# Performance work log

Measured on AMD Instinct MI355X. Metric: run time of the kernel, lower is better.

## Reference

```python
import jax, jax.numpy as jnp
import numpy as np

D_MODEL = 1024
H = 16
D_K = 64
D_V = 64
NEG_INF = -1e9
LN_EPS = 1e-5


def setup_inputs() -> dict:
    key = jax.random.key(0)
    ks = jax.random.split(key, 7)
    B, S = 4, 2048
    scale = 1.0 / np.sqrt(D_MODEL)
    return {
        "Q": jax.random.normal(ks[0], (B, S, D_MODEL), jnp.float32),
        "K": jax.random.normal(ks[1], (B, S, D_MODEL), jnp.float32),
        "V": jax.random.normal(ks[2], (B, S, D_MODEL), jnp.float32),
        "W_Q": jax.random.normal(ks[3], (D_MODEL, D_K * H), jnp.float32) * scale,
        "W_K": jax.random.normal(ks[4], (D_MODEL, D_K * H), jnp.float32) * scale,
        "W_V": jax.random.normal(ks[5], (D_MODEL, D_V * H), jnp.float32) * scale,
        "W_O": jax.random.normal(ks[6], (D_V * H, D_MODEL), jnp.float32) * scale,
        "ln_gamma": jnp.ones((D_MODEL,), jnp.float32),
        "ln_beta": jnp.zeros((D_MODEL,), jnp.float32),
    }


def reference(Q, K, V, W_Q, W_K, W_V, W_O, ln_gamma, ln_beta):
    B, Lq, _ = Q.shape
    Lk = K.shape[1]
    # projections, split into heads: [B, H, L, d]
    Qh = (Q @ W_Q).reshape(B, Lq, H, D_K).transpose(0, 2, 1, 3)
    Kh = (K @ W_K).reshape(B, Lk, H, D_K).transpose(0, 2, 1, 3)
    Vh = (V @ W_V).reshape(B, Lk, H, D_V).transpose(0, 2, 1, 3)
    # scaled dot-product scores [B, H, Lq, Lk]
    scores = jnp.einsum("bhqd,bhkd->bhqk", Qh, Kh) / jnp.sqrt(jnp.float32(D_K))
    # causal mask: upper triangle (excl. diagonal) gets -1e9 added
    mask = jnp.triu(jnp.full((Lq, Lk), NEG_INF, jnp.float32), k=1)
    scores = scores + mask
    attn = jax.nn.softmax(scores, axis=-1)
    ctx = jnp.einsum("bhqk,bhkd->bhqd", attn, Vh)
    ctx = ctx.transpose(0, 2, 1, 3).reshape(B, Lq, H * D_V)
    out = ctx @ W_O
    # residual + layernorm
    x = Q + out
    mu = jnp.mean(x, axis=-1, keepdims=True)
    var = jnp.mean(jnp.square(x - mu), axis=-1, keepdims=True)
    return (x - mu) * jax.lax.rsqrt(var + LN_EPS) * ln_gamma + ln_beta
```

## Files before the change

kernel.cpp:

```cpp
#include <hip/hip_runtime.h>
#include <cstdint>
#include <cstddef>

#define DM  1024
#define SEQ 2048
#define BATCH 4
#define NH  16
#define DH  64
#define QKS 2048

typedef __bf16 bf16_t;
typedef __bf16 bf16x8 __attribute__((ext_vector_type(8)));
typedef __bf16 bf16x4 __attribute__((ext_vector_type(4)));
typedef float  f32x4  __attribute__((ext_vector_type(4)));

#define MFMA16(a, b, c) __builtin_amdgcn_mfma_f32_16x16x32_bf16((a), (b), (c), 0, 0, 0)

#define CS 0.18033688f

#define ASYNC_COPY16(gsrc, ldst)                                                   \
  __builtin_amdgcn_global_load_lds(                                                \
      (__attribute__((address_space(1))) void*)(gsrc),                             \
      (__attribute__((address_space(3))) void*)(ldst), 16, 0, 0)

#define NCVT (3 * BATCH * SEQ * DM / 4 / 256)

__global__ __launch_bounds__(256) void prep_kernel(const float* __restrict__ Q,
                                                   const float* __restrict__ K,
                                                   const float* __restrict__ V,
                                                   const float* __restrict__ W0,
                                                   const float* __restrict__ W1,
                                                   const float* __restrict__ W2,
                                                   const float* __restrict__ W3,
                                                   bf16_t* __restrict__ Qb,
                                                   bf16_t* __restrict__ Kb,
                                                   bf16_t* __restrict__ Vb,
                                                   bf16_t* __restrict__ WTall) {
  __shared__ float tile[32][33];
  const int bid = blockIdx.x;
  if (bid < NCVT) {
    const int n4 = BATCH * SEQ * DM / 4;
    int i = bid * 256 + threadIdx.x;
    const float* src; bf16_t* dst; int j;
    if (i < n4)           { src = Q; dst = Qb; j = i; }
    else if (i < 2 * n4)  { src = K; dst = Kb; j = i - n4; }
    else                  { src = V; dst = Vb; j = i - 2 * n4; }
    float4 v = ((const float4*)src)[j];
    bf16x4 o;
    o[0] = (bf16_t)v.x; o[1] = (bf16_t)v.y; o[2] = (bf16_t)v.z; o[3] = (bf16_t)v.w;
    *(bf16x4*)(dst + (size_t)j * 4) = o;
    return;
  }
  const int wb = bid - NCVT;
  const int widx = wb >> 10, wid = wb & 1023;
  const float* W = (widx == 0) ? W0 : (widx == 1) ? W1 : (widx == 2) ? W2 : W3;
  bf16_t* WT = WTall + (size_t)widx * DM * DM;
  const int bn = wid & 31, bk = wid >> 5;
  const int tx = threadIdx.x & 31, ty = threadIdx.x >> 5;
#pragma unroll
  for (int r = 0; r < 4; ++r)
    tile[ty + r * 8][tx] = W[(size_t)(bk * 32 + ty + r * 8) * DM + bn * 32 + tx];
  __syncthreads();
#pragma unroll
  for (int r = 0; r < 4; ++r)
    WT[(size_t)(bn * 32 + ty + r * 8) * DM + bk * 32 + tx] = (bf16_t)tile[tx][ty + r * 8];
}

__global__ __launch_bounds__(256) void gemm_bt_kernel(const bf16_t* __restrict__ A0,
                                                      const bf16_t* __restrict__ A1,
                                                      const bf16_t* __restrict__ A2,
                                                      const bf16_t* __restrict__ BT,
                                                      bf16_t* __restrict__ C,
                                                      bf16_t* __restrict__ Vtr,
                                                      int K, int ldc,
                                                      float qscale, int qcols) {
  __shared__ bf16_t Sh[4][128 * 32];
  const int tid = threadIdx.x;
  const int wv = tid >> 6, lane = tid & 63;
  const int lo = lane & 15, quad = lane >> 4;

  const int bid = blockIdx.x;
  const int xcd = bid & 7;
  const int rid = bid >> 3;
  const int m0 = (xcd * 8 + (rid & 7)) * 128;
  const int n0 = (rid >> 3) * 128;
  const int wm = wv & 1, wn = wv >> 1;

  const bf16_t* A = (n0 < 1024) ? A0 : (n0 < 2048) ? A1 : A2;
  const float sc = (n0 < qcols) ? qscale : 1.0f;

  f32x4 acc[4][4] = {};

  const int srow = wv * 32 + (lane >> 2);
  const int scol = (lane & 3) * 8;
  const bf16_t* Ag = A + (size_t)(m0 + srow) * K + scol;
  const bf16_t* Bg = BT + (size_t)(n0 + srow) * K + scol;
  const int lds_off = (wv * 32) * 32;

  ASYNC_COPY16(Ag, Sh[0] + lds_off);
  ASYNC_COPY16(Ag + (size_t)16 * K, Sh[0] + lds_off + 16 * 32);
  ASYNC_COPY16(Bg, Sh[2] + lds_off);
  ASYNC_COPY16(Bg + (size_t)16 * K, Sh[2] + lds_off + 16 * 32);

  const int kiters = K >> 5;
  for (int ki = 0; ki < kiters; ++ki) {
    const int cur = ki & 1;
    __syncthreads();
    if (ki + 1 < kiters) {
      const int k1 = (ki + 1) << 5;
      ASYNC_COPY16(Ag + k1, Sh[cur ^ 1] + lds_off);
      ASYNC_COPY16(Ag + k1 + (size_t)16 * K, Sh[cur ^ 1] + lds_off + 16 * 32);
      ASYNC_COPY16(Bg + k1, Sh[2 + (cur ^ 1)] + lds_off);
      ASYNC_COPY16(Bg + k1 + (size_t)16 * K, Sh[2 + (cur ^ 1)] + lds_off + 16 * 32);
    }

    bf16x8 af[4], bfr[4];
#pragma unroll
    for (int t = 0; t < 4; ++t) {
      af[t]  = *(const bf16x8*)(Sh[cur] + (wm * 64 + t * 16 + lo) * 32 + quad * 8);
      bfr[t] = *(const bf16x8*)(Sh[2 + cur] + (wn * 64 + t * 16 + lo) * 32 + quad * 8);
    }
#pragma unroll
    for (int mt = 0; mt < 4; ++mt)
#pragma unroll
      for (int nt = 0; nt < 4; ++nt)
        acc[mt][nt] = MFMA16(af[mt], bfr[nt], acc[mt][nt]);
  }

  __syncthreads();

  if (Vtr != nullptr && n0 >= 2048) {
    bf16_t* Tw = &Sh[wv][0];
#pragma unroll
    for (int nt = 0; nt < 4; ++nt) {
      const int row = nt * 16 + lo;
#pragma unroll
      for (int mt = 0; mt < 4; ++mt) {
        const int cb = mt * 16 + quad * 4;
        bf16x4 pk;
#pragma unroll
        for (int r = 0; r < 4; ++r) pk[r] = (bf16_t)acc[mt][nt][r];
        *(bf16x4*)(Tw + row * 64 + (((cb >> 3) ^ (row & 7)) * 8) + (cb & 7)) = pk;
      }
    }
    __asm__ volatile("s_waitcnt lgkmcnt(0)" ::: "memory");
    const int h  = ((n0 - 2048) >> 6) + wn;
    const int mg = m0 + wm * 64;
    const int b  = mg >> 11;
    const int s0 = mg & (SEQ - 1);
    const int dr = lane >> 3, ck = lane & 7;
    bf16_t* vbase = Vtr + ((size_t)((b * NH + h) * DH)) * SEQ + s0;
#pragma unroll
    for (int pass = 0; pass < 8; ++pass) {
      const int d = pass * 8 + dr;
      const bf16x8 vv = *(const bf16x8*)(Tw + d * 64 + ((ck ^ (d & 7)) * 8));
      *(bf16x8*)(vbase + (size_t)d * SEQ + ck * 8) = vv;
    }
    return;
  }

#pragma unroll
  for (int mt = 0; mt < 4; ++mt)
#pragma unroll
    for (int nt = 0; nt < 4; ++nt)
#pragma unroll
      for (int r = 0; r < 4; ++r) {
        const int m = m0 + wm * 64 + mt * 16 + quad * 4 + r;
        const int n = n0 + wn * 64 + nt * 16 + lo;
        C[(size_t)m * ldc + n] = (bf16_t)(acc[mt][nt][r] * sc);
      }
}

__global__ __launch_bounds__(256) void attn_kernel(const bf16_t* __restrict__ QKV,
                                                   const bf16_t* __restrict__ Vt,
                                                   bf16_t* __restrict__ ctx) {
  __shared__ bf16_t Ks[2][64 * 64];
  __shared__ bf16_t Vs[2][64 * 64];
  __shared__ bf16_t Ps[4][16 * 64];
  const int tid = threadIdx.x;
  const int wv = tid >> 6, lane = tid & 63;
  const int lo = lane & 15, quad = lane >> 4;
  const int bh = blockIdx.x & 63;
  const int pid = blockIdx.x >> 6;
  const int b = bh >> 4, h = bh & 15;

  const bf16_t* Qg = QKV + ((size_t)b * SEQ) * QKS + h * DH;
  const bf16_t* Kg = QKV + ((size_t)b * SEQ) * QKS + 1024 + h * DH;
  const bf16_t* Vg = Vt + ((size_t)(bh * DH)) * SEQ;

  const int U0 = wv * 128 + lane, U1 = U0 + 64;
  const int r0 = U0 >> 3, cg0 = (U0 & 7) ^ (r0 & 7);
  const int r1 = U1 >> 3, cg1 = (U1 & 7) ^ (r1 & 7);

  bf16_t* Pw = &Ps[wv][0];

  for (int half = 0; half < 2; ++half) {
    const int qblk = half ? (31 - pid) : pid;
    const int qw0 = qblk * 64 + wv * 16;
    const int qg = qw0 + lo;

    const bf16_t* Qb = Qg + ((size_t)(qw0 + lo)) * QKS + quad * 8;
    const bf16x8 aQ0 = *(const bf16x8*)(Qb);
    const bf16x8 aQ1 = *(const bf16x8*)(Qb + 32);

    f32x4 O[4] = {};
    float l_run = 0.0f;

    __syncthreads();
    ASYNC_COPY16(Kg + (size_t)r0 * QKS + cg0 * 8, Ks[0] + (wv * 2 + 0) * 512);
    ASYNC_COPY16(Kg + (size_t)r1 * QKS + cg1 * 8, Ks[0] + (wv * 2 + 1) * 512);
    ASYNC_COPY16(Vg + (size_t)r0 * SEQ + cg0 * 8, Vs[0] + (wv * 2 + 0) * 512);
    ASYNC_COPY16(Vg + (size_t)r1 * SEQ + cg1 * 8, Vs[0] + (wv * 2 + 1) * 512);

    for (int jt = 0; jt <= qblk; ++jt) {
      const int cur = jt & 1;
      __syncthreads();
      if (jt < qblk) {
        const int j1 = (jt + 1) * 64;
        ASYNC_COPY16(Kg + (size_t)(j1 + r0) * QKS + cg0 * 8, Ks[cur ^ 1] + (wv * 2 + 0) * 512);
        ASYNC_COPY16(Kg + (size_t)(j1 + r1) * QKS + cg1 * 8, Ks[cur ^ 1] + (wv * 2 + 1) * 512);
        ASYNC_COPY16(Vg + (size_t)r0 * SEQ + j1 + cg0 * 8, Vs[cur ^ 1] + (wv * 2 + 0) * 512);
        ASYNC_COPY16(Vg + (size_t)r1 * SEQ + j1 + cg1 * 8, Vs[cur ^ 1] + (wv * 2 + 1) * 512);
      }

      const int j0 = jt * 64;
      f32x4 st[4];
#pragma unroll
      for (int mt = 0; mt < 4; ++mt) {
        const int row = mt * 16 + lo;
        const bf16x8 k0 = *(const bf16x8*)(Ks[cur] + row * 64 + ((quad ^ (row & 7)) * 8));
        const bf16x8 k1 = *(const bf16x8*)(Ks[cur] + row * 64 + (((4 + quad) ^ (row & 7)) * 8));
        f32x4 s = {};
        s = MFMA16(k0, aQ0, s);
        s = MFMA16(k1, aQ1, s);
        st[mt] = s;
      }

      float lsum = 0.0f;
      const bool diag = (jt == qblk);
#pragma unroll
      for (int mt = 0; mt < 4; ++mt) {
        bf16x4 pk;
#pragma unroll
        for (int r = 0; r < 4; ++r) {
          float s = st[mt][r];
          if (diag && (j0 + mt * 16 + quad * 4 + r > qg)) s = -1e30f;
          const float p = __builtin_amdgcn_exp2f(s);
          lsum += p;
          pk[r] = (bf16_t)p;
        }
        const int sp = (mt * 2 + (quad >> 1)) ^ (lo & 7);
        *(bf16x4*)(Pw + lo * 64 + sp * 8 + (quad & 1) * 4) = pk;
      }
      lsum += __shfl_xor(lsum, 16);
      lsum += __shfl_xor(lsum, 32);
      l_run += lsum;

      __asm__ volatile("s_waitcnt lgkmcnt(0)" ::: "memory");
      const bf16x8 p0 = *(const bf16x8*)(Pw + lo * 64 + ((quad ^ (lo & 7)) * 8));
      const bf16x8 p1 = *(const bf16x8*)(Pw + lo * 64 + (((4 + quad) ^ (lo & 7)) * 8));
#pragma unroll
      for (int nt = 0; nt < 4; ++nt) {
        const int row = nt * 16 + lo;
        const bf16x8 v0 = *(const bf16x8*)(Vs[cur] + row * 64 + ((quad ^ (row & 7)) * 8));
        const bf16x8 v1 = *(const bf16x8*)(Vs[cur] + row * 64 + (((4 + quad) ^ (row & 7)) * 8));
        O[nt] = MFMA16(p0, v0, O[nt]);
        O[nt] = MFMA16(p1, v1, O[nt]);
      }
    }

    float inv[4];
#pragma unroll
    for (int r = 0; r < 4; ++r) inv[r] = 1.0f / __shfl(l_run, quad * 4 + r);
    bf16_t* outp = ctx + ((size_t)(b * SEQ + qw0 + quad * 4)) * DM + h * DH + lo;
#pragma unroll
    for (int r = 0; r < 4; ++r)
#pragma unroll
      for (int nt = 0; nt < 4; ++nt)
        outp[(size_t)r * DM + nt * 16] = (bf16_t)(O[nt][r] * inv[r]);
  }
}

__global__ __launch_bounds__(256) void ln_kernel(const float* __restrict__ Qin,
                                                 const bf16_t* __restrict__ Y,
                                                 const float* __restrict__ gamma,
                                                 const float* __restrict__ beta,
                                                 float* __restrict__ out) {
  const int row = blockIdx.x, t = threadIdx.x;
  const float4 a = ((const float4*)(Qin + (size_t)row * DM))[t];
  const bf16x4 yv = ((const bf16x4*)(Y + (size_t)row * DM))[t];
  const float x0 = a.x + (float)yv[0], x1 = a.y + (float)yv[1];
  const float x2 = a.z + (float)yv[2], x3 = a.w + (float)yv[3];
  float s  = x0 + x1 + x2 + x3;
  float ss = x0 * x0 + x1 * x1 + x2 * x2 + x3 * x3;
#pragma unroll
  for (int off = 1; off < 64; off <<= 1) { s += __shfl_xor(s, off); ss += __shfl_xor(ss, off); }
  __shared__ float red[8];
  const int wv = t >> 6, lane = t & 63;
  if (lane == 0) { red[wv * 2] = s; red[wv * 2 + 1] = ss; }
  __syncthreads();
  s  = red[0] + red[2] + red[4] + red[6];
  ss = red[1] + red[3] + red[5] + red[7];
  const float mu  = s * (1.0f / DM);
  const float var = ss * (1.0f / DM) - mu * mu;
  const float rstd = rsqrtf(var + 1e-5f);
  const float4 g  = ((const float4*)gamma)[t];
  const float4 be = ((const float4*)beta)[t];
  float4 o;
  o.x = (x0 - mu) * rstd * g.x + be.x;
  o.y = (x1 - mu) * rstd * g.y + be.y;
  o.z = (x2 - mu) * rstd * g.z + be.z;
  o.w = (x3 - mu) * rstd * g.w + be.w;
  ((float4*)(out + (size_t)row * DM))[t] = o;
}

extern "C" void kernel_launch(void* const* d_in, const int* in_sizes, int n_in,
                              void* d_out, int out_size, void* d_ws, size_t ws_size,
                              hipStream_t stream) {
  const float* Q     = (const float*)d_in[0];
  const float* K     = (const float*)d_in[1];
  const float* V     = (const float*)d_in[2];
  const float* W_Q   = (const float*)d_in[3];
  const float* W_K   = (const float*)d_in[4];
  const float* W_V   = (const float*)d_in[5];
  const float* W_O   = (const float*)d_in[6];
  const float* gamma = (const float*)d_in[7];
  const float* beta  = (const float*)d_in[8];
  float* out = (float*)d_out;

  char* ws = (char*)d_ws;
  const size_t SZB = (size_t)BATCH * SEQ * DM * 2;
  const size_t WTB = (size_t)DM * DM * 2;
  bf16_t* Qb    = (bf16_t*)(ws);
  bf16_t* Kb    = (bf16_t*)(ws + SZB);
  bf16_t* Vb    = (bf16_t*)(ws + 2 * SZB);
  bf16_t* Yb    = (bf16_t*)(ws);
  bf16_t* WTall = (bf16_t*)(ws + 3 * SZB);
  char* p2 = ws + 3 * SZB + 4 * WTB;
  bf16_t* QKV = (bf16_t*)(p2);
  bf16_t* Vtr = (bf16_t*)(p2 + 2 * SZB);
  bf16_t* ctx = (bf16_t*)(p2 + 3 * SZB);

  prep_kernel<<<NCVT + 4096, 256, 0, stream>>>(Q, K, V, W_Q, W_K, W_V, W_O,
                                               Qb, Kb, Vb, WTall);

  gemm_bt_kernel<<<(3072 / 128) * (BATCH * SEQ / 128), 256, 0, stream>>>(
      Qb, Kb, Vb, WTall, QKV, Vtr, DM, QKS, CS, 1024);

  attn_kernel<<<64 * 16, 256, 0, stream>>>(QKV, Vtr, ctx);

  gemm_bt_kernel<<<(DM / 128) * (BATCH * SEQ / 128), 256, 0, stream>>>(
      ctx, ctx, ctx, WTall + (size_t)3 * DM * DM, Yb, nullptr, DM, DM, 1.0f, 0);
  ln_kernel<<<BATCH * SEQ, 256, 0, stream>>>(Q, Yb, gamma, beta, out);
}
```

Before: 316.3 us.

## Process two 64-row query blocks per workgroup to reuse K/V tiles

Each workgroup now handles 128 query rows, as two 64-row sub-blocks A and B, instead of 64. Every K/V tile loaded into LDS therefore serves both sub-blocks, roughly halving K/V global and LDS traffic per query. The grid is halved to 512 blocks, with causal balancing pairing qblk and 15-qblk. The cost is more registers (two Q fragments and two accumulator sets), fewer blocks for occupancy and load balance, and a wasted half-step on the last tile where only B is active.

Result: no change. 314.3 us (-0.6%).

```diff
diff --git a/kernel.cpp b/kernel.cpp
--- a/kernel.cpp
+++ b/kernel.cpp
@@ -176,7 +176,7 @@
                                                    bf16_t* __restrict__ ctx) {
   __shared__ bf16_t Ks[2][64 * 64];
   __shared__ bf16_t Vs[2][64 * 64];
-  __shared__ bf16_t Ps[4][16 * 64];
+  __shared__ bf16_t Ps[4][2][16 * 64];
   const int tid = threadIdx.x;
   const int wv = tid >> 6, lane = tid & 63;
   const int lo = lane & 15, quad = lane >> 4;
@@ -192,19 +192,28 @@
   const int r0 = U0 >> 3, cg0 = (U0 & 7) ^ (r0 & 7);
   const int r1 = U1 >> 3, cg1 = (U1 & 7) ^ (r1 & 7);
 
-  bf16_t* Pw = &Ps[wv][0];
+  bf16_t* PwA = &Ps[wv][0][0];
+  bf16_t* PwB = &Ps[wv][1][0];
+  const int pwr_base = lo * 64;
+  const int prd0 = lo * 64 + ((quad ^ (lo & 7)) * 8);
+  const int prd1 = lo * 64 + (((4 + quad) ^ (lo & 7)) * 8);
 
   for (int half = 0; half < 2; ++half) {
-    const int qblk = half ? (31 - pid) : pid;
-    const int qw0 = qblk * 64 + wv * 16;
-    const int qg = qw0 + lo;
-
-    const bf16_t* Qb = Qg + ((size_t)(qw0 + lo)) * QKS + quad * 8;
-    const bf16x8 aQ0 = *(const bf16x8*)(Qb);
-    const bf16x8 aQ1 = *(const bf16x8*)(Qb + 32);
-
-    f32x4 O[4] = {};
-    float l_run = 0.0f;
+    const int qblk = half ? (15 - pid) : pid;
+    const int jmax = 2 * qblk + 1;
+    const int qw = qblk * 128 + wv * 16;
+    const int qgA = qw + lo;
+    const int qgB = qgA + 64;
+
+    const bf16_t* Qba = Qg + ((size_t)qgA) * QKS + quad * 8;
+    const bf16x8 aQ0A = *(const bf16x8*)(Qba);
+    const bf16x8 aQ1A = *(const bf16x8*)(Qba + 32);
+    const bf16_t* Qbb = Qba + (size_t)64 * QKS;
+    const bf16x8 aQ0B = *(const bf16x8*)(Qbb);
+    const bf16x8 aQ1B = *(const bf16x8*)(Qbb + 32);
+
+    f32x4 OA[4] = {}, OB[4] = {};
+    float lA = 0.0f, lB = 0.0f;
 
     __syncthreads();
     ASYNC_COPY16(Kg + (size_t)r0 * QKS + cg0 * 8, Ks[0] + (wv * 2 + 0) * 512);
@@ -212,72 +221,121 @@
     ASYNC_COPY16(Vg + (size_t)r0 * SEQ + cg0 * 8, Vs[0] + (wv * 2 + 0) * 512);
     ASYNC_COPY16(Vg + (size_t)r1 * SEQ + cg1 * 8, Vs[0] + (wv * 2 + 1) * 512);
 
-    for (int jt = 0; jt <= qblk; ++jt) {
-      const int cur = jt & 1;
-      __syncthreads();
-      if (jt < qblk) {
-        const int j1 = (jt + 1) * 64;
-        ASYNC_COPY16(Kg + (size_t)(j1 + r0) * QKS + cg0 * 8, Ks[cur ^ 1] + (wv * 2 + 0) * 512);
-        ASYNC_COPY16(Kg + (size_t)(j1 + r1) * QKS + cg1 * 8, Ks[cur ^ 1] + (wv * 2 + 1) * 512);
-        ASYNC_COPY16(Vg + (size_t)r0 * SEQ + j1 + cg0 * 8, Vs[cur ^ 1] + (wv * 2 + 0) * 512);
-        ASYNC_COPY16(Vg + (size_t)r1 * SEQ + j1 + cg1 * 8, Vs[cur ^ 1] + (wv * 2 + 1) * 512);
+    for (int jtp = 0; jtp <= jmax; jtp += 2) {
+#pragma unroll
+      for (int u = 0; u < 2; ++u) {
+        const int jt = jtp + u;
+        __syncthreads();
+        if (jt < jmax) {
+          const int j1 = (jt + 1) * 64;
+          ASYNC_COPY16(Kg + (size_t)(j1 + r0) * QKS + cg0 * 8, Ks[u ^ 1] + (wv * 2 + 0) * 512);
+          ASYNC_COPY16(Kg + (size_t)(j1 + r1) * QKS + cg1 * 8, Ks[u ^ 1] + (wv * 2 + 1) * 512);
+          ASYNC_COPY16(Vg + (size_t)r0 * SEQ + j1 + cg0 * 8, Vs[u ^ 1] + (wv * 2 + 0) * 512);
+          ASYNC_COPY16(Vg + (size_t)r1 * SEQ + j1 + cg1 * 8, Vs[u ^ 1] + (wv * 2 + 1) * 512);
+        }
+
+        const int j0 = jt * 64;
+        const bool aact = (jt != jmax);
+        const bool diagA = (jt == jmax - 1);
+        const bool diagB = (jt == jmax);
+
+        f32x4 sA[4], sB[4];
+#pragma unroll
+        for (int mt = 0; mt < 4; ++mt) {
+          const int row = mt * 16 + lo;
+          const bf16x8 k0 = *(const bf16x8*)(Ks[u] + row * 64 + ((quad ^ (row & 7)) * 8));
+          const bf16x8 k1 = *(const bf16x8*)(Ks[u] + row * 64 + (((4 + quad) ^ (row & 7)) * 8));
+          if (aact) {
+            f32x4 s = {};
+            s = MFMA16(k0, aQ0A, s);
+            s = MFMA16(k1, aQ1A, s);
+            sA[mt] = s;
+          }
+          f32x4 t = {};
+          t = MFMA16(k0, aQ0B, t);
+          t = MFMA16(k1, aQ1B, t);
+          sB[mt] = t;
+        }
+
+        if (aact) {
+          float ls = 0.0f;
+#pragma unroll
+          for (int mt = 0; mt < 4; ++mt) {
+            bf16x4 pk;
+#pragma unroll
+            for (int r = 0; r < 4; ++r) {
+              float s = sA[mt][r];
+              if (diagA && (j0 + mt * 16 + quad * 4 + r > qgA)) s = -1e30f;
+              const float p = __builtin_amdgcn_exp2f(s);
+              ls += p;
+              pk[r] = (bf16_t)p;
+            }
+            const int sp = (mt * 2 + (quad >> 1)) ^ (lo & 7);
+            *(bf16x4*)(PwA + pwr_base + sp * 8 + (quad & 1) * 4) = pk;
+          }
+          ls += __shfl_xor(ls, 16);
+          ls += __shfl_xor(ls, 32);
+          lA += ls;
+        }
+        {
+          float ls = 0.0f;
+#pragma unroll
+          for (int mt = 0; mt < 4; ++mt) {
+            bf16x4 pk;
+#pragma unroll
+            for (int r = 0; r < 4; ++r) {
+              float s = sB[mt][r];
+              if (diagB && (j0 + mt * 16 + quad * 4 + r > qgB)) s = -1e30f;
+              const float p = __builtin_amdgcn_exp2f(s);
+              ls += p;
+              pk[r] = (bf16_t)p;
+            }
+            const int sp = (mt * 2 + (quad >> 1)) ^ (lo & 7);
+            *(bf16x4*)(PwB + pwr_base + sp * 8 + (quad & 1) * 4) = pk;
+          }
+          ls += __shfl_xor(ls, 16);
+          ls += __shfl_xor(ls, 32);
+          lB += ls;
+        }
+
+        __asm__ volatile("s_waitcnt lgkmcnt(0)" ::: "memory");
+        bf16x8 pA0, pA1;
+        if (aact) {
+          pA0 = *(const bf16x8*)(PwA + prd0);
+          pA1 = *(const bf16x8*)(PwA + prd1);
+        }
+        const bf16x8 pB0 = *(const bf16x8*)(PwB + prd0);
+        const bf16x8 pB1 = *(const bf16x8*)(PwB + prd1);
+
+#pragma unroll
+        for (int nt = 0; nt < 4; ++nt) {
+          const int row = nt * 16 + lo;
+          const bf16x8 v0 = *(const bf16x8*)(Vs[u] + row * 64 + ((quad ^ (row & 7)) * 8));
+          const bf16x8 v1 = *(const bf16x8*)(Vs[u] + row * 64 + (((4 + quad) ^ (row & 7)) * 8));
+          if (aact) {
+            OA[nt] = MFMA16(pA0, v0, OA[nt]);
+            OA[nt] = MFMA16(pA1, v1, OA[nt]);
+          }
+          OB[nt] = MFMA16(pB0, v0, OB[nt]);
+          OB[nt] = MFMA16(pB1, v1, OB[nt]);
+        }
       }
-
-      const int j0 = jt * 64;
-      f32x4 st[4];
-#pragma unroll
-      for (int mt = 0; mt < 4; ++mt) {
-        const int row = mt * 16 + lo;
-        const bf16x8 k0 = *(const bf16x8*)(Ks[cur] + row * 64 + ((quad ^ (row & 7)) * 8));
-        const bf16x8 k1 = *(const bf16x8*)(Ks[cur] + row * 64 + (((4 + quad) ^ (row & 7)) * 8));
-        f32x4 s = {};
-        s = MFMA16(k0, aQ0, s);
-        s = MFMA16(k1, aQ1, s);
-        st[mt] = s;
+    }
+
+    float invA[4], invB[4];
+#pragma unroll
+    for (int r = 0; r < 4; ++r) {
+      invA[r] = 1.0f / __shfl(lA, quad * 4 + r);
+      invB[r] = 1.0f / __shfl(lB, quad * 4 + r);
+    }
+    bf16_t* outp = ctx + ((size_t)(b * SEQ + qw + quad * 4)) * DM + h * DH + lo;
+#pragma unroll
+    for (int r = 0; r < 4; ++r)
+#pragma unroll
+      for (int nt = 0; nt < 4; ++nt) {
+        outp[(size_t)r * DM + nt * 16] = (bf16_t)(OA[nt][r] * invA[r]);
+        outp[(size_t)(r + 64) * DM + nt * 16] = (bf16_t)(OB[nt][r] * invB[r]);
       }
-
-      float lsum = 0.0f;
-      const bool diag = (jt == qblk);
-#pragma unroll
-      for (int mt = 0; mt < 4; ++mt) {
-        bf16x4 pk;
-#pragma unroll
-        for (int r = 0; r < 4; ++r) {
-          float s = st[mt][r];
-          if (diag && (j0 + mt * 16 + quad * 4 + r > qg)) s = -1e30f;
-          const float p = __builtin_amdgcn_exp2f(s);
-          lsum += p;
-          pk[r] = (bf16_t)p;
-        }
-        const int sp = (mt * 2 + (quad >> 1)) ^ (lo & 7);
-        *(bf16x4*)(Pw + lo * 64 + sp * 8 + (quad & 1) * 4) = pk;
-      }
-      lsum += __shfl_xor(lsum, 16);
-      lsum += __shfl_xor(lsum, 32);
-      l_run += lsum;
-
-      __asm__ volatile("s_waitcnt lgkmcnt(0)" ::: "memory");
-      const bf16x8 p0 = *(const bf16x8*)(Pw + lo * 64 + ((quad ^ (lo & 7)) * 8));
-      const bf16x8 p1 = *(const bf16x8*)(Pw + lo * 64 + (((4 + quad) ^ (lo & 7)) * 8));
-#pragma unroll
-      for (int nt = 0; nt < 4; ++nt) {
-        const int row = nt * 16 + lo;
-        const bf16x8 v0 = *(const bf16x8*)(Vs[cur] + row * 64 + ((quad ^ (row & 7)) * 8));
-        const bf16x8 v1 = *(const bf16x8*)(Vs[cur] + row * 64 + (((4 + quad) ^ (row & 7)) * 8));
-        O[nt] = MFMA16(p0, v0, O[nt]);
-        O[nt] = MFMA16(p1, v1, O[nt]);
-      }
-    }
-
-    float inv[4];
-#pragma unroll
-    for (int r = 0; r < 4; ++r) inv[r] = 1.0f / __shfl(l_run, quad * 4 + r);
-    bf16_t* outp = ctx + ((size_t)(b * SEQ + qw0 + quad * 4)) * DM + h * DH + lo;
-#pragma unroll
-    for (int r = 0; r < 4; ++r)
-#pragma unroll
-      for (int nt = 0; nt < 4; ++nt)
-        outp[(size_t)r * DM + nt * 16] = (bf16_t)(O[nt][r] * inv[r]);
   }
 }
 
@@ -347,7 +405,7 @@
   gemm_bt_kernel<<<(3072 / 128) * (BATCH * SEQ / 128), 256, 0, stream>>>(
       Qb, Kb, Vb, WTall, QKV, Vtr, DM, QKS, CS, 1024);
 
-  attn_kernel<<<64 * 16, 256, 0, stream>>>(QKV, Vtr, ctx);
+  attn_kernel<<<64 * 8, 256, 0, stream>>>(QKV, Vtr, ctx);
 
   gemm_bt_kernel<<<(DM / 128) * (BATCH * SEQ / 128), 256, 0, stream>>>(
       ctx, ctx, ctx, WTall + (size_t)3 * DM * DM, Yb, nullptr, DM, DM, 1.0f, 0);
```
